# Kernel optimization log

Measured on AMD Instinct MI355X. Metric: run time of the kernel, lower is better.

The kernel has to match this reference:

```python
import jax, jax.numpy as jnp
import numpy as np

N, T, F = 16, 4096, 256
PROP = 0.3
TP = T + 2 * int(PROP * T)  # static max padded length (pad_i <= floor(PROP*T))


def setup_inputs() -> dict:
    key = jax.random.key(0)
    k1, k2, k3 = jax.random.split(key, 3)
    in_ = jax.random.normal(k1, (N, T, F), dtype=jnp.float32)
    in_lens = jax.random.randint(k2, (N,), 1, T + 1)  # lens in [1, T]
    # torch: pad = (prop * lens) * rand, then .long()  (floor)
    u = jax.random.uniform(k3, (2, N))
    pad = jnp.floor(PROP * in_lens[None, :].astype(jnp.float32) * u).astype(jnp.int32)
    return {"in_": in_, "in_lens": in_lens, "pad": pad}


def reference(in_, in_lens, pad):
    # reflect-mode variable pad: out[n, t] = in_[n, src(n, t)] for t < out_lens[n]
    n, t_dim, f = in_.shape
    t = jnp.arange(TP)  # (TP,)
    pad0 = pad[0][:, None]  # (N,1)
    pad1 = pad[1][:, None]
    lens = in_lens[:, None].astype(jnp.int32)
    # left reflect: src = pad0 - t; middle: src = t - pad0;
    # right reflect (r = t - pad0 - lens): src = lens - r - 2
    left_src = jnp.clip(pad0 - t, 0, t_dim - 1)
    mid_src = jnp.clip(t - pad0, 0, t_dim - 1)
    right_src = jnp.clip(2 * lens + pad0 - t - 2, 0, t_dim - 1)
    src = jnp.where(t < pad0, left_src,
                    jnp.where(t < pad0 + lens, mid_src, right_src))  # (N,TP)
    out = jnp.take_along_axis(in_, src[:, :, None], axis=1)  # (N,TP,F)
    out_lens = in_lens + pad.sum(0)
    valid = (t[None, :] < out_lens[:, None])[:, :, None]
    out = jnp.where(valid, out, jnp.zeros((), dtype=in_.dtype))
    return out, out_lens
```

## Files before the change

kernel.cpp:

```cpp
#include <hip/hip_runtime.h>


#define N_  16
#define T_  4096
#define F_  256
#define TP_ 6552
#define F4_ (F_ / 4)

__global__ __launch_bounds__(256) void random_shift_kernel(
    const float* __restrict__ in_,
    const int*   __restrict__ in_lens,
    const int*   __restrict__ pad,
    float*       __restrict__ out)
{
    const int i = blockIdx.x * blockDim.x + threadIdx.x;

    if (i < N_) {
        const int len = in_lens[i];
        const int ol  = len + pad[i] + pad[N_ + i];
        out[(size_t)N_ * TP_ * F_ + i] = (float)ol;
    }

    const int total = N_ * TP_ * F4_;
    if (i >= total) return;

    const int f4  = i & (F4_ - 1);
    const int row = i >> 6;
    const int t   = row % TP_;
    const int n   = row / TP_;

    const int pad0 = pad[n];
    const int pad1 = pad[N_ + n];
    const int len  = in_lens[n];
    const int out_len = len + pad0 + pad1;

    float4 v = make_float4(0.f, 0.f, 0.f, 0.f);
    if (t < out_len) {
        int src;
        if (t < pad0)             src = pad0 - t;
        else if (t < pad0 + len)  src = t - pad0;
        else                      src = 2 * len + pad0 - t - 2;
        src = min(max(src, 0), T_ - 1);
        const float4* inrow =
            (const float4*)(in_ + ((size_t)n * T_ + src) * F_);
        v = inrow[f4];
    }
    ((float4*)out)[i] = v;
}

extern "C" void kernel_launch(void* const* d_in, const int* in_sizes, int n_in,
                              void* d_out, int out_size, void* d_ws, size_t ws_size,
                              hipStream_t stream) {
    const float* in_     = (const float*)d_in[0];
    const int*   in_lens = (const int*)d_in[1];
    const int*   pad     = (const int*)d_in[2];
    float*       out     = (float*)d_out;

    const int total  = N_ * TP_ * F4_;
    const int block  = 256;
    const int grid   = (total + block - 1) / block;
    random_shift_kernel<<<grid, block, 0, stream>>>(in_, in_lens, pad, out);
}
```

Before: 148.3 us.

## Process multiple rows per wave with batched loads and nontemporal stores

Restructures the launch to a 2D grid (row blocks by batch), with each wave handling six consecutive output rows. Per-batch parameters are loaded once per block, all six loads are issued before the stores, and fully padded row groups write zeros without reading input. Stores use nontemporal hints so output does not pollute the cache. The clamp on src is removed, so correctness relies on the pad bound assumptions holding.

```diff
diff --git a/kernel.cpp b/kernel.cpp
--- a/kernel.cpp
+++ b/kernel.cpp
@@ -7,45 +7,65 @@
 #define TP_ 6552
 #define F4_ (F_ / 4)
 
+#define RPW 6
+#define RPB (RPW * 4)
+#define GX  (TP_ / RPB)
+
+typedef float v4f __attribute__((ext_vector_type(4)));
+
 __global__ __launch_bounds__(256) void random_shift_kernel(
     const float* __restrict__ in_,
     const int*   __restrict__ in_lens,
     const int*   __restrict__ pad,
     float*       __restrict__ out)
 {
-    const int i = blockIdx.x * blockDim.x + threadIdx.x;
+    const int n = blockIdx.y;
+    const int pad0 = pad[n];
+    const int len  = in_lens[n];
+    const int out_len = len + pad0 + pad[N_ + n];
 
-    if (i < N_) {
-        const int len = in_lens[i];
-        const int ol  = len + pad[i] + pad[N_ + i];
-        out[(size_t)N_ * TP_ * F_ + i] = (float)ol;
+    if (blockIdx.x == 0 && threadIdx.x == 0)
+        out[(size_t)N_ * TP_ * F_ + n] = (float)out_len;
+
+    const int lane = threadIdx.x & 63;
+    const int wave = threadIdx.x >> 6;
+    const int t0   = blockIdx.x * RPB + wave * RPW;
+
+    const v4f* __restrict__ inb  = (const v4f*)(in_ + (size_t)n * T_ * F_);
+    v4f*       __restrict__ outb = (v4f*)(out + (size_t)n * TP_ * F_);
+
+    if (t0 + RPW <= out_len) {
+        v4f vv[RPW];
+        #pragma unroll
+        for (int r = 0; r < RPW; ++r) {
+            const int t = t0 + r;
+            const int src = (t < pad0)       ? (pad0 - t)
+                          : (t < pad0 + len) ? (t - pad0)
+                          :                    (2 * len + pad0 - t - 2);
+            vv[r] = inb[(size_t)src * F4_ + lane];
+        }
+        #pragma unroll
+        for (int r = 0; r < RPW; ++r)
+            __builtin_nontemporal_store(vv[r], &outb[(size_t)(t0 + r) * F4_ + lane]);
+    } else if (t0 >= out_len) {
+        const v4f z = (v4f){0.f, 0.f, 0.f, 0.f};
+        #pragma unroll
+        for (int r = 0; r < RPW; ++r)
+            __builtin_nontemporal_store(z, &outb[(size_t)(t0 + r) * F4_ + lane]);
+    } else {
+        #pragma unroll
+        for (int r = 0; r < RPW; ++r) {
+            const int t = t0 + r;
+            v4f v = (v4f){0.f, 0.f, 0.f, 0.f};
+            if (t < out_len) {
+                const int src = (t < pad0)       ? (pad0 - t)
+                              : (t < pad0 + len) ? (t - pad0)
+                              :                    (2 * len + pad0 - t - 2);
+                v = inb[(size_t)src * F4_ + lane];
+            }
+            __builtin_nontemporal_store(v, &outb[(size_t)t * F4_ + lane]);
+        }
     }
-
-    const int total = N_ * TP_ * F4_;
-    if (i >= total) return;
-
-    const int f4  = i & (F4_ - 1);
-    const int row = i >> 6;
-    const int t   = row % TP_;
-    const int n   = row / TP_;
-
-    const int pad0 = pad[n];
-    const int pad1 = pad[N_ + n];
-    const int len  = in_lens[n];
-    const int out_len = len + pad0 + pad1;
-
-    float4 v = make_float4(0.f, 0.f, 0.f, 0.f);
-    if (t < out_len) {
-        int src;
-        if (t < pad0)             src = pad0 - t;
-        else if (t < pad0 + len)  src = t - pad0;
-        else                      src = 2 * len + pad0 - t - 2;
-        src = min(max(src, 0), T_ - 1);
-        const float4* inrow =
-            (const float4*)(in_ + ((size_t)n * T_ + src) * F_);
-        v = inrow[f4];
-    }
-    ((float4*)out)[i] = v;
 }
 
 extern "C" void kernel_launch(void* const* d_in, const int* in_sizes, int n_in,
@@ -56,8 +76,6 @@
     const int*   pad     = (const int*)d_in[2];
     float*       out     = (float*)d_out;
 
-    const int total  = N_ * TP_ * F4_;
-    const int block  = 256;
-    const int grid   = (total + block - 1) / block;
-    random_shift_kernel<<<grid, block, 0, stream>>>(in_, in_lens, pad, out);
+    dim3 grid(GX, N_);
+    random_shift_kernel<<<grid, dim3(256), 0, stream>>>(in_, in_lens, pad, out);
 }
```

After: 155.8 us. 1.05x slower.
